# Optimization experiments

Measured on AMD Instinct MI355X. Metric: run time of the kernel, lower is better.

The kernel has to match this reference:

```python
import jax, jax.numpy as jnp
import numpy as np

D = 1024      # model_dim
H = 16        # num_heads
DH = D // H   # depth per head
F = 4096      # ffn_dim
B, L = 4, 2048
LN_EPS = 1e-5


def layer_norm(x, g, b):
    mu = jnp.mean(x, axis=-1, keepdims=True)
    var = jnp.var(x, axis=-1, keepdims=True)
    return (x - mu) * jax.lax.rsqrt(var + LN_EPS) * g + b


def setup_inputs() -> dict:
    key = jax.random.key(0)
    ks = jax.random.split(key, 12)
    s = 0.02
    return {
        "inputs": jax.random.normal(ks[0], (B, L, D), jnp.float32),
        "Wq": jax.random.normal(ks[1], (D, D), jnp.float32) * s,
        "Wk": jax.random.normal(ks[2], (D, D), jnp.float32) * s,
        "Wv": jax.random.normal(ks[3], (D, D), jnp.float32) * s,
        "Wo": jax.random.normal(ks[4], (D, D), jnp.float32) * s,
        "W1": jax.random.normal(ks[5], (F, D), jnp.float32) * s,
        "b1": jnp.zeros((F,), jnp.float32),
        "W2": jax.random.normal(ks[6], (D, F), jnp.float32) * s,
        "b2": jnp.zeros((D,), jnp.float32),
        "ln_g": jnp.ones((D,), jnp.float32),
        "ln_b": jnp.zeros((D,), jnp.float32),
    }


def reference(inputs, Wq, Wk, Wv, Wo, W1, b1, W2, b2, ln_g, ln_b):
    # --- MultiHeadAttention (faithful to source, incl. the bug where
    # ScaledDotProductAttention returns v, not attention @ v) ---
    scale = DH ** -0.5
    q = (inputs @ Wq.T) * scale            # [B,L,D], scaled before head split
    k = inputs @ Wk.T                      # [B,L,D]
    v = inputs @ Wv.T                      # [B,L,D]
    # only the LAST head's attention scores survive the python loop
    qH = q[..., (H - 1) * DH:]             # [B,L,DH]
    kH = k[..., (H - 1) * DH:]             # [B,L,DH]
    attn = jax.nn.softmax(jnp.einsum('bqd,bkd->bqk', qH, kH), axis=-1) / H
    # combine_heads(split_heads(v)) == v, so context = Wo applied to v
    context = v @ Wo.T                     # [B,L,D]; dropout(p=0) is identity

    # --- PositionalWiseFeedForward: conv1d(kernel=1) == pointwise linear ---
    h = jax.nn.relu(context @ W1.T + b1)   # [B,L,F]
    ffn = h @ W2.T + b2                    # [B,L,D]
    out = layer_norm(context + ffn, ln_g, ln_b)
    return out, attn
```

## Files before the change

kernel.cpp:

```cpp
#include <hip/hip_runtime.h>
#include <hip/hip_bf16.h>
#include <stdint.h>

#define D_ 1024
#define H_ 16
#define DH_ 64
#define F_ 4096
#define B_ 4
#define L_ 2048
#define MTOK 8192

typedef __attribute__((ext_vector_type(8))) short bf16x8;
typedef __attribute__((ext_vector_type(4))) float f32x4;

__device__ __forceinline__ short f2bf(float f) {
  uint32_t u = __float_as_uint(f);
  uint32_t r = (u + 0x7FFFu + ((u >> 16) & 1u)) >> 16;
  return (short)(uint16_t)r;
}
__device__ __forceinline__ float bf2f(short s) {
  return __uint_as_float(((uint32_t)(uint16_t)s) << 16);
}

__device__ __forceinline__ void gload_lds16(const short* g, short* l) {
  __builtin_amdgcn_global_load_lds(
      (const __attribute__((address_space(1))) void*)g,
      (__attribute__((address_space(3))) void*)l,
      16, 0, 0);
}

#define FENCE asm volatile("" ::: "memory")
#define BARX  do { FENCE; __builtin_amdgcn_s_barrier(); FENCE; } while (0)
#define PRIO1 __builtin_amdgcn_s_setprio(1)
#define PRIO0 __builtin_amdgcn_s_setprio(0)

__global__ void __launch_bounds__(256) convert_all(
    const float* __restrict__ Wq, const float* __restrict__ Wk,
    const float* __restrict__ Wv, const float* __restrict__ Wo,
    const float* __restrict__ W1, const float* __restrict__ W2,
    const float* __restrict__ inputs,
    short* __restrict__ wqk, short* __restrict__ wv, short* __restrict__ wo,
    short* __restrict__ w1, short* __restrict__ w2, short* __restrict__ in_bf) {
  long i = ((long)blockIdx.x * 256 + threadIdx.x) * 4;
  const float* src; short* dst; long off; float scale = 1.0f;
  if (i < 65536L)        { src = Wq + 960L * 1024; dst = wqk;         off = i;            scale = 0.125f; }
  else if (i < 131072L)  { src = Wk + 960L * 1024; dst = wqk + 65536; off = i - 65536L;   }
  else if (i < 1179648L) { src = Wv;     dst = wv;    off = i - 131072L;   }
  else if (i < 2228224L) { src = Wo;     dst = wo;    off = i - 1179648L;  }
  else if (i < 6422528L) { src = W1;     dst = w1;    off = i - 2228224L;  }
  else if (i < 10616832L){ src = W2;     dst = w2;    off = i - 6422528L;  }
  else                   { src = inputs; dst = in_bf; off = i - 10616832L; }
  float4 f = *(const float4*)(src + off);
  short4 o4;
  o4.x = f2bf(f.x * scale); o4.y = f2bf(f.y * scale);
  o4.z = f2bf(f.z * scale); o4.w = f2bf(f.w * scale);
  *(short4*)(dst + off) = o4;
}

__global__ void __launch_bounds__(256) transpose_bf16_1k(
    const short* __restrict__ src, short* __restrict__ dst) {
  __shared__ short t[64][65];
  const int bx = blockIdx.x, by = blockIdx.y;
  const int lr = threadIdx.x >> 4;
  const int lc = (threadIdx.x & 15) * 4;
#pragma unroll
  for (int rr = 0; rr < 4; rr++) {
    int r = lr * 4 + rr;
    short4 v = *(const short4*)&src[(long)(by * 64 + r) * 1024 + bx * 64 + lc];
    t[r][lc] = v.x; t[r][lc + 1] = v.y; t[r][lc + 2] = v.z; t[r][lc + 3] = v.w;
  }
  __syncthreads();
#pragma unroll
  for (int rr = 0; rr < 4; rr++) {
    int r = lr * 4 + rr;
    short4 v;
    v.x = t[lc + 0][r]; v.y = t[lc + 1][r];
    v.z = t[lc + 2][r]; v.w = t[lc + 3][r];
    *(short4*)&dst[(long)(bx * 64 + r) * 1024 + by * 64 + lc] = v;
  }
}


#define RD_A(mh_, par_) do {                                                  \
  const short* bp = lds + (par_) * BUF + wm * ASLOT;                          \
  _Pragma("unroll")                                                           \
  for (int m2 = 0; m2 < MH; m2++) {                                           \
    const int r = ((mh_) * MH + m2) * 16 + l15;                               \
    _Pragma("unroll")                                                         \
    for (int ks = 0; ks < 2; ks++)                                            \
      aF[mh_][m2][ks] =                                                       \
          *(const bf16x8*)(bp + r * 64 + (((ks * 4 + l4) ^ (r & 7)) << 3));   \
  } } while (0)

#define RD_B(nh_, par_) do {                                                  \
  const short* bp = lds + (par_) * BUF + BM * 64 + (wn >> 1) * 8192;          \
  _Pragma("unroll")                                                           \
  for (int n2 = 0; n2 < 2; n2++) {                                            \
    const int r = (wn & 1) * 64 + ((nh_) * 2 + n2) * 16 + l15;                \
    _Pragma("unroll")                                                         \
    for (int ks = 0; ks < 2; ks++)                                            \
      bF[nh_][n2][ks] =                                                       \
          *(const bf16x8*)(bp + r * 64 + (((ks * 4 + l4) ^ (r & 7)) << 3));   \
  } } while (0)

#define QUAD(mh_, nh_) do {                                                   \
  _Pragma("unroll")                                                           \
  for (int ks = 0; ks < 2; ks++)                                              \
    _Pragma("unroll")                                                         \
    for (int m2 = 0; m2 < MH; m2++)                                           \
      _Pragma("unroll")                                                       \
      for (int n2 = 0; n2 < 2; n2++)                                          \
        acc[(mh_) * MH + m2][(nh_) * 2 + n2] =                                \
            __builtin_amdgcn_mfma_f32_16x16x32_bf16(                          \
                aF[mh_][m2][ks], bF[nh_][n2][ks],                             \
                acc[(mh_) * MH + m2][(nh_) * 2 + n2], 0, 0, 0);               \
} while (0)

#define ITER2(g_, par_, SN, SPP, GK) do {                                     \
     \
  RD_B(0, par_); RD_A(0, par_); RD_B(1, par_);                                \
  if (SN) stA((g_) + 1, 1, (par_) ^ 1);                                       \
  PRIO1; QUAD(0, 0); QUAD(0, 1); PRIO0;                                       \
  BARX;           \
                                                                 \
  RD_A(1, par_);                                                              \
  if (SPP) { stB((g_) + 2, 0, par_); stB((g_) + 2, 1, par_);                  \
             stA((g_) + 2, 0, par_); }                                        \
  PRIO1; QUAD(1, 0); QUAD(1, 1); PRIO0;                                       \
  if (GK == 1) asm volatile("s_waitcnt vmcnt(%0)" :: "i"(VG) : "memory");     \
  else if (GK == 2) asm volatile("s_waitcnt vmcnt(0)" ::: "memory");          \
  BARX;                         \
} while (0)

template<int BMT, bool BIAS, bool RELU>
__global__ void __launch_bounds__(512, 2) gemm8p(
    const short* __restrict__ A, int lda,
    const short* __restrict__ Bm, int ldb,
    short* __restrict__ C, int ldc,
    const float* __restrict__ bias, int K) {
  constexpr int BM = BMT * 128;
  constexpr int MT = BMT * 4;
  constexpr int MH = MT / 2;
  constexpr int LA = BMT;
  constexpr int LB = 2;
  constexpr int ASLOT = (BM / 2) * 64;
  constexpr int BUF = BM * 64 + 16384;
  constexpr int VG = 2 * LB + LA;

  __shared__ __align__(16) short lds[2 * BUF];

  const int tid = threadIdx.x;
  const int lane = tid & 63;
  const int wave = tid >> 6;
  const int wm = wave >> 2, wn = wave & 3;
  const int l15 = lane & 15, l4 = lane >> 4;

  const int id = blockIdx.y * gridDim.x + blockIdx.x;
  const int per = (gridDim.x * gridDim.y) >> 3;
  const int swz = (id & 7) * per + (id >> 3);
  const int bn = swz % gridDim.x;
  const int bm = swz / gridDim.x;

  const short* Ab = A + (long)bm * BM * lda;
  const short* Bb = Bm + (long)bn * 256 * ldb;
  const int NTILE = K >> 6;

  const short* gA[2][LA]; short* dA[2][LA];
  const short* gB[2][LB]; short* dB[2][LB];
#pragma unroll
  for (int h = 0; h < 2; h++) {
#pragma unroll
    for (int l = 0; l < LA; l++) {
      int c = l * 512 + tid, r = c >> 3, cg = (c & 7) ^ (r & 7);
      gA[h][l] = Ab + (long)(h * (BM / 2) + r) * lda + cg * 8;
      dA[h][l] = lds + h * ASLOT + c * 8;
    }
#pragma unroll
    for (int l = 0; l < LB; l++) {
      int c = l * 512 + tid, r = c >> 3, cg = (c & 7) ^ (r & 7);
      gB[h][l] = Bb + (long)(h * 128 + r) * ldb + cg * 8;
      dB[h][l] = lds + BM * 64 + h * 8192 + c * 8;
    }
  }
  auto stA = [&](int t, int h, int par) {
#pragma unroll
    for (int l = 0; l < LA; l++)
      gload_lds16(gA[h][l] + (t << 6), dA[h][l] + par * BUF);
  };
  auto stB = [&](int t, int h, int par) {
#pragma unroll
    for (int l = 0; l < LB; l++)
      gload_lds16(gB[h][l] + (t << 6), dB[h][l] + par * BUF);
  };

  f32x4 acc[MT][4];
#pragma unroll
  for (int i = 0; i < MT; i++)
#pragma unroll
    for (int j = 0; j < 4; j++) acc[i][j] = (f32x4){0.f, 0.f, 0.f, 0.f};

  bf16x8 aF[2][MH][2];
  bf16x8 bF[2][2][2];

  stA(0, 0, 0); stA(0, 1, 0); stB(0, 0, 0); stB(0, 1, 0);
  stB(1, 0, 1); stB(1, 1, 1); stA(1, 0, 1);
  asm volatile("s_waitcnt vmcnt(%0)" :: "i"(VG) : "memory");
  BARX;

  for (int g = 0; g + 3 < NTILE; g += 2) {
    ITER2(g, 0, 1, 1, 1);
    ITER2(g + 1, 1, 1, 1, 1);
  }
  ITER2(NTILE - 2, 0, 1, 0, 2);
  ITER2(NTILE - 1, 1, 0, 0, 0);

  short* epi = lds + wave * 4608;
  const int col0 = bn * 256 + wn * 64;
  const int row0 = bm * BM + wm * (BM / 2);
  const int rg = lane >> 3, sg = lane & 7;
  float bb[4];
#pragma unroll
  for (int nt = 0; nt < 4; nt++)
    bb[nt] = BIAS ? bias[col0 + nt * 16 + l15] : 0.f;
#pragma unroll
  for (int h = 0; h < BMT; h++) {
#pragma unroll
    for (int m2 = 0; m2 < 4; m2++) {
#pragma unroll
      for (int nt = 0; nt < 4; nt++) {
#pragma unroll
        for (int r = 0; r < 4; r++) {
          float v = acc[h * 4 + m2][nt][r] + bb[nt];
          if (RELU) v = v > 0.f ? v : 0.f;
          epi[(m2 * 16 + l4 * 4 + r) * 72 + nt * 16 + l15] = f2bf(v);
        }
      }
    }
    FENCE;
#pragma unroll
    for (int it = 0; it < 8; it++) {
      const int rl = it * 8 + rg;
      bf16x8 vv = *(const bf16x8*)(epi + rl * 72 + sg * 8);
      *(bf16x8*)(C + (long)(row0 + h * 64 + rl) * ldc + col0 + sg * 8) = vv;
    }
    FENCE;
  }
}

__global__ void __launch_bounds__(256) gemm_small(
    const short* __restrict__ in_bf, const short* __restrict__ wqk,
    short* __restrict__ qkh,
    const short* __restrict__ wo, const short* __restrict__ wvT,
    short* __restrict__ wf) {
  const short* A; const short* Bm; short* C;
  int ldc, bn, bm;
  const int bid = blockIdx.x;
  if (bid < 64) { A = in_bf; Bm = wqk; C = qkh; ldc = 128; bn = 0; bm = bid; }
  else { A = wo; Bm = wvT; C = wf; ldc = 1024; int b2 = bid - 64; bn = b2 & 7; bm = b2 >> 3; }
  const int lda = 1024, ldb = 1024, K = 1024;

  const short* Ab = A + (long)bm * 128 * lda;
  const short* Bb = Bm + (long)bn * 128 * ldb;

  __shared__ short lA[128 * 64];
  __shared__ short lB[128 * 64];

  const int tid = threadIdx.x;
  const int lane = tid & 63;
  const int wave = tid >> 6;
  const int wr = wave >> 1, wc = wave & 1;

  f32x4 acc[4][4];
#pragma unroll
  for (int i = 0; i < 4; i++)
#pragma unroll
    for (int j = 0; j < 4; j++) acc[i][j] = (f32x4){0.f, 0.f, 0.f, 0.f};

  for (int k0 = 0; k0 < K; k0 += 64) {
    __syncthreads();
#pragma unroll
    for (int i = 0; i < 4; i++) {
      int c = i * 256 + tid;
      int row = c >> 3;
      int col = (c & 7) * 8;
      gload_lds16(Ab + (long)row * lda + k0 + col, &lA[c * 8]);
      gload_lds16(Bb + (long)row * ldb + k0 + col, &lB[c * 8]);
    }
    __syncthreads();

#pragma unroll
    for (int ks = 0; ks < 2; ks++) {
      bf16x8 af[4], bfr[4];
#pragma unroll
      for (int t = 0; t < 4; t++) {
        af[t]  = *(const bf16x8*)&lA[(wr * 64 + t * 16 + (lane & 15)) * 64 + ks * 32 + (lane >> 4) * 8];
        bfr[t] = *(const bf16x8*)&lB[(wc * 64 + t * 16 + (lane & 15)) * 64 + ks * 32 + (lane >> 4) * 8];
      }
#pragma unroll
      for (int mt = 0; mt < 4; mt++)
#pragma unroll
        for (int nt = 0; nt < 4; nt++)
          acc[mt][nt] = __builtin_amdgcn_mfma_f32_16x16x32_bf16(af[mt], bfr[nt], acc[mt][nt], 0, 0, 0);
    }
  }

  const int col0 = bn * 128 + wc * 64;
  const int row0 = bm * 128 + wr * 64;
#pragma unroll
  for (int mt = 0; mt < 4; mt++) {
#pragma unroll
    for (int nt = 0; nt < 4; nt++) {
      int col = col0 + nt * 16 + (lane & 15);
      int rbase = row0 + mt * 16 + (lane >> 4) * 4;
#pragma unroll
      for (int r = 0; r < 4; r++)
        C[(long)(rbase + r) * ldc + col] = f2bf(acc[mt][nt][r]);
    }
  }
}

__global__ void __launch_bounds__(512) fused_attn(
    const short* __restrict__ qkh, float* __restrict__ attn) {
  const int tid = threadIdx.x;
  const int lane = tid & 63;
  const int wave = tid >> 6;
  const int l15 = lane & 15, l4 = lane >> 4;
  const int b = blockIdx.y;
  const int q0 = blockIdx.x * 16;
  const long base = (long)b * 2048;

  bf16x8 qf[2];
#pragma unroll
  for (int ks = 0; ks < 2; ks++)
    qf[ks] = *(const bf16x8*)&qkh[(base + q0 + l15) * 128 + ks * 32 + l4 * 8];

  const short* kb = qkh + (base + (long)wave * 256) * 128 + 64;

  f32x4 s[16];
#pragma unroll
  for (int kt = 0; kt < 16; kt++) {
    bf16x8 kf0 = *(const bf16x8*)&kb[(kt * 16 + l15) * 128 + l4 * 8];
    bf16x8 kf1 = *(const bf16x8*)&kb[(kt * 16 + l15) * 128 + 32 + l4 * 8];
    f32x4 a = (f32x4){0.f, 0.f, 0.f, 0.f};
    a = __builtin_amdgcn_mfma_f32_16x16x32_bf16(kf0, qf[0], a, 0, 0, 0);
    a = __builtin_amdgcn_mfma_f32_16x16x32_bf16(kf1, qf[1], a, 0, 0, 0);
    s[kt] = a;
  }

  float m = -1e30f;
#pragma unroll
  for (int kt = 0; kt < 16; kt++)
    m = fmaxf(m, fmaxf(fmaxf(s[kt][0], s[kt][1]), fmaxf(s[kt][2], s[kt][3])));
#pragma unroll
  for (int o = 16; o <= 32; o <<= 1) m = fmaxf(m, __shfl_xor(m, o, 64));

  float ss = 0.f;
#pragma unroll
  for (int kt = 0; kt < 16; kt++) {
    f32x4 e;
#pragma unroll
    for (int r = 0; r < 4; r++) e[r] = __expf(s[kt][r] - m);
    s[kt] = e;
    ss += (e[0] + e[1]) + (e[2] + e[3]);
  }
#pragma unroll
  for (int o = 16; o <= 32; o <<= 1) ss += __shfl_xor(ss, o, 64);

  __shared__ float lm[8][16], lsm[8][16];
  if (lane < 16) { lm[wave][l15] = m; lsm[wave][l15] = ss; }
  __syncthreads();
  float M = -1e30f;
#pragma unroll
  for (int w2 = 0; w2 < 8; w2++) M = fmaxf(M, lm[w2][l15]);
  float S = 0.f;
#pragma unroll
  for (int w2 = 0; w2 < 8; w2++) S += lsm[w2][l15] * __expf(lm[w2][l15] - M);
  const float f = __expf(m - M) / (S * 16.0f);

  float* attb = attn + (base + q0 + l15) * 2048 + wave * 256 + l4 * 4;
#pragma unroll
  for (int kt = 0; kt < 16; kt++) {
    f32x4 p;
#pragma unroll
    for (int r = 0; r < 4; r++) p[r] = s[kt][r] * f;
    *(f32x4*)(attb + kt * 16) = p;
  }
}

__device__ __forceinline__ float wave_sum(float v) {
#pragma unroll
  for (int o = 32; o > 0; o >>= 1) v += __shfl_xor(v, o, 64);
  return v;
}

__global__ void __launch_bounds__(256) ln_fuse(
    const short* __restrict__ ctx, const short* __restrict__ ffn,
    const float* __restrict__ g, const float* __restrict__ bta,
    float* __restrict__ out) {
  const int tid = threadIdx.x;
  long base = (long)blockIdx.x * 1024 + tid * 4;
  short4 c4 = *(const short4*)(ctx + base);
  short4 f4 = *(const short4*)(ffn + base);
  float x0 = bf2f(c4.x) + bf2f(f4.x);
  float x1 = bf2f(c4.y) + bf2f(f4.y);
  float x2 = bf2f(c4.z) + bf2f(f4.z);
  float x3 = bf2f(c4.w) + bf2f(f4.w);

  float s = (x0 + x1) + (x2 + x3);
  float q = (x0 * x0 + x1 * x1) + (x2 * x2 + x3 * x3);
  __shared__ float rs[4], rq[4];
  s = wave_sum(s);
  q = wave_sum(q);
  if ((tid & 63) == 0) { rs[tid >> 6] = s; rq[tid >> 6] = q; }
  __syncthreads();
  float S = rs[0] + rs[1] + rs[2] + rs[3];
  float Q = rq[0] + rq[1] + rq[2] + rq[3];
  float mu = S * (1.0f / 1024.0f);
  float var = Q * (1.0f / 1024.0f) - mu * mu;
  float inv = rsqrtf(var + 1e-5f);

  float4 g4 = *(const float4*)(g + tid * 4);
  float4 b4 = *(const float4*)(bta + tid * 4);
  float4 o;
  o.x = (x0 - mu) * inv * g4.x + b4.x;
  o.y = (x1 - mu) * inv * g4.y + b4.y;
  o.z = (x2 - mu) * inv * g4.z + b4.z;
  o.w = (x3 - mu) * inv * g4.w + b4.w;
  *(float4*)(out + base) = o;
}

extern "C" void kernel_launch(void* const* d_in, const int* in_sizes, int n_in,
                              void* d_out, int out_size, void* d_ws, size_t ws_size,
                              hipStream_t stream) {
  const float* inputs = (const float*)d_in[0];
  const float* Wq = (const float*)d_in[1];
  const float* Wk = (const float*)d_in[2];
  const float* Wv = (const float*)d_in[3];
  const float* Wo = (const float*)d_in[4];
  const float* W1 = (const float*)d_in[5];
  const float* b1 = (const float*)d_in[6];
  const float* W2 = (const float*)d_in[7];
  const float* b2 = (const float*)d_in[8];
  const float* ln_g = (const float*)d_in[9];
  const float* ln_b = (const float*)d_in[10];

  char* w = (char*)d_ws;
  short* in_bf = (short*)w;  w += (long)MTOK * D_ * 2;
  short* wqk   = (short*)w;  w += 128L * D_ * 2;
  short* wv    = (short*)w;  w += (long)D_ * D_ * 2;
  short* wo    = (short*)w;  w += (long)D_ * D_ * 2;
  short* w1    = (short*)w;  w += (long)F_ * D_ * 2;
  short* w2    = (short*)w;  w += (long)D_ * F_ * 2;
  short* qkh   = (short*)w;  w += (long)MTOK * 128 * 2;
  short* wvT   = (short*)w;  w += (long)D_ * D_ * 2;
  short* wf    = (short*)w;  w += (long)D_ * D_ * 2;
  short* ctxbf = (short*)w;  w += (long)MTOK * D_ * 2;
  short* hbf   = (short*)w;  w += (long)MTOK * F_ * 2;
  short* ffnbf = (short*)w;  w += (long)MTOK * D_ * 2;

  float* out  = (float*)d_out;
  float* attn = out + (long)MTOK * D_;

  convert_all<<<dim3(18560), 256, 0, stream>>>(
      Wq, Wk, Wv, Wo, W1, W2, inputs, wqk, wv, wo, w1, w2, in_bf);

  transpose_bf16_1k<<<dim3(16, 16), 256, 0, stream>>>(wv, wvT);
  gemm_small<<<dim3(128), 256, 0, stream>>>(in_bf, wqk, qkh, wo, wvT, wf);

  fused_attn<<<dim3(128, 4), 512, 0, stream>>>(qkh, attn);
  gemm8p<1, false, false><<<dim3(4, 64), 512, 0, stream>>>(
      in_bf, D_, wf, D_, ctxbf, D_, nullptr, D_);
  gemm8p<2, true, true><<<dim3(16, 32), 512, 0, stream>>>(
      ctxbf, D_, w1, D_, hbf, F_, b1, D_);
  gemm8p<1, true, false><<<dim3(4, 64), 512, 0, stream>>>(
      hbf, F_, w2, F_, ffnbf, D_, b2, F_);
  ln_fuse<<<dim3(MTOK), 256, 0, stream>>>(ctxbf, ffnbf, ln_g, ln_b, out);
}
```

Measured before the change: 241.9 us.

## Add triple-buffered 128x256 GEMM kernel for the FFN up-projection

Introduces a new GEMM kernel with 128x256 tiles, a K-step of 32, a three-stage LDS ring buffer and launch bounds targeting 4 blocks per CU. The grid is swizzled across groups of 8 blocks for better L2 locality. It replaces the 256x256 double-buffered kernel for the W1 GEMM with bias and ReLU. The aim is higher occupancy and deeper load/compute overlap, at the cost of a smaller per-block tile and less register reuse per MFMA.

```diff
diff --git a/kernel.cpp b/kernel.cpp
--- a/kernel.cpp
+++ b/kernel.cpp
@@ -117,19 +117,17 @@
 } while (0)
 
 #define ITER2(g_, par_, SN, SPP, GK) do {                                     \
-     \
   RD_B(0, par_); RD_A(0, par_); RD_B(1, par_);                                \
   if (SN) stA((g_) + 1, 1, (par_) ^ 1);                                       \
   PRIO1; QUAD(0, 0); QUAD(0, 1); PRIO0;                                       \
-  BARX;           \
-                                                                 \
+  BARX;                                                                       \
   RD_A(1, par_);                                                              \
   if (SPP) { stB((g_) + 2, 0, par_); stB((g_) + 2, 1, par_);                  \
              stA((g_) + 2, 0, par_); }                                        \
   PRIO1; QUAD(1, 0); QUAD(1, 1); PRIO0;                                       \
   if (GK == 1) asm volatile("s_waitcnt vmcnt(%0)" :: "i"(VG) : "memory");     \
   else if (GK == 2) asm volatile("s_waitcnt vmcnt(0)" ::: "memory");          \
-  BARX;                         \
+  BARX;                                                                       \
 } while (0)
 
 template<int BMT, bool BIAS, bool RELU>
@@ -247,6 +245,124 @@
   }
 }
 
+template<bool BIAS, bool RELU>
+__global__ void __launch_bounds__(512, 4) gemm_t3(
+    const short* __restrict__ A, int lda,
+    const short* __restrict__ Bm, int ldb,
+    short* __restrict__ C, int ldc,
+    const float* __restrict__ bias, int K) {
+  constexpr int ABUF = 4096;
+  constexpr int BUF  = 12288;
+  __shared__ __align__(16) short lds[3 * BUF];
+
+  const int tid = threadIdx.x;
+  const int lane = tid & 63;
+  const int wave = tid >> 6;
+  const int wm = wave >> 2, wn = wave & 3;
+  const int l15 = lane & 15, l4 = lane >> 4;
+
+  const int id = blockIdx.y * gridDim.x + blockIdx.x;
+  const int per = (gridDim.x * gridDim.y) >> 3;
+  const int swz = (id & 7) * per + (id >> 3);
+  const int bn = swz % gridDim.x;
+  const int bm = swz / gridDim.x;
+
+  const short* Ab = A + (long)bm * 128 * lda;
+  const short* Bb = Bm + (long)bn * 256 * ldb;
+  const int NTILE = K >> 5;
+
+  const short* gA0; int dOfA;
+  {
+    int c = tid, r = c >> 2, kg = (c & 3) ^ (r & 3);
+    gA0 = Ab + (long)r * lda + kg * 8;
+    dOfA = c * 8;
+  }
+  const short* gB[2]; int dOfB[2];
+#pragma unroll
+  for (int l = 0; l < 2; l++) {
+    int c = l * 512 + tid, r = c >> 2, kg = (c & 3) ^ (r & 3);
+    gB[l] = Bb + (long)r * ldb + kg * 8;
+    dOfB[l] = ABUF + c * 8;
+  }
+  auto stage = [&](int t, int pS) {
+    const int k0 = t << 5;
+    gload_lds16(gA0 + k0, lds + pS + dOfA);
+#pragma unroll
+    for (int l = 0; l < 2; l++) gload_lds16(gB[l] + k0, lds + pS + dOfB[l]);
+  };
+
+  int aOf[4], bOf[4];
+#pragma unroll
+  for (int t = 0; t < 4; t++) {
+    int ra = wm * 64 + t * 16 + l15;
+    int rb = wn * 64 + t * 16 + l15;
+    aOf[t] = (ra * 4 + (l4 ^ (ra & 3))) * 8;
+    bOf[t] = ABUF + (rb * 4 + (l4 ^ (rb & 3))) * 8;
+  }
+
+  f32x4 acc[4][4];
+#pragma unroll
+  for (int i = 0; i < 4; i++)
+#pragma unroll
+    for (int j = 0; j < 4; j++) acc[i][j] = (f32x4){0.f, 0.f, 0.f, 0.f};
+
+  stage(0, 0); stage(1, BUF);
+  asm volatile("s_waitcnt vmcnt(3)" ::: "memory");
+  BARX;
+
+  int p0 = 0, p1 = BUF, p2 = 2 * BUF;
+  for (int g = 0; g < NTILE; g++) {
+    bf16x8 aF[4], bF[4];
+#pragma unroll
+    for (int t = 0; t < 4; t++) aF[t] = *(const bf16x8*)(lds + p0 + aOf[t]);
+#pragma unroll
+    for (int t = 0; t < 4; t++) bF[t] = *(const bf16x8*)(lds + p0 + bOf[t]);
+    if (g + 2 < NTILE) stage(g + 2, p2);
+    PRIO1;
+#pragma unroll
+    for (int mt = 0; mt < 4; mt++)
+#pragma unroll
+      for (int nt = 0; nt < 4; nt++)
+        acc[mt][nt] = __builtin_amdgcn_mfma_f32_16x16x32_bf16(
+            aF[mt], bF[nt], acc[mt][nt], 0, 0, 0);
+    PRIO0;
+    if (g + 2 < NTILE)
+      asm volatile("s_waitcnt vmcnt(3)" ::: "memory");
+    else if (g + 1 < NTILE)
+      asm volatile("s_waitcnt vmcnt(0)" ::: "memory");
+    BARX;
+    int tmp = p0; p0 = p1; p1 = p2; p2 = tmp;
+  }
+
+  short* epi = lds + wave * 4608;
+  const int col0 = bn * 256 + wn * 64;
+  const int row0 = bm * 128 + wm * 64;
+  const int rg = lane >> 3, sg = lane & 7;
+  float bb[4];
+#pragma unroll
+  for (int nt = 0; nt < 4; nt++)
+    bb[nt] = BIAS ? bias[col0 + nt * 16 + l15] : 0.f;
+#pragma unroll
+  for (int m2 = 0; m2 < 4; m2++) {
+#pragma unroll
+    for (int nt = 0; nt < 4; nt++) {
+#pragma unroll
+      for (int r = 0; r < 4; r++) {
+        float v = acc[m2][nt][r] + bb[nt];
+        if (RELU) v = v > 0.f ? v : 0.f;
+        epi[(m2 * 16 + l4 * 4 + r) * 72 + nt * 16 + l15] = f2bf(v);
+      }
+    }
+  }
+  FENCE;
+#pragma unroll
+  for (int it = 0; it < 8; it++) {
+    const int rl = it * 8 + rg;
+    bf16x8 vv = *(const bf16x8*)(epi + rl * 72 + sg * 8);
+    *(bf16x8*)(C + (long)(row0 + rl) * ldc + col0 + sg * 8) = vv;
+  }
+}
+
 __global__ void __launch_bounds__(256) gemm_small(
     const short* __restrict__ in_bf, const short* __restrict__ wqk,
     short* __restrict__ qkh,
@@ -470,7 +586,7 @@
   fused_attn<<<dim3(128, 4), 512, 0, stream>>>(qkh, attn);
   gemm8p<1, false, false><<<dim3(4, 64), 512, 0, stream>>>(
       in_bf, D_, wf, D_, ctxbf, D_, nullptr, D_);
-  gemm8p<2, true, true><<<dim3(16, 32), 512, 0, stream>>>(
+  gemm_t3<true, true><<<dim3(16, 64), 512, 0, stream>>>(
       ctxbf, D_, w1, D_, hbf, F_, b1, D_);
   gemm8p<1, true, false><<<dim3(4, 64), 512, 0, stream>>>(
       hbf, F_, w2, F_, ffnbf, D_, b2, F_);
```

Measured after the change: 254.7 us. +5.3%, slower.
